# Kernel tuning notes

Hardware: AMD Instinct MI355X
Metric: run time of the kernel (lower is better)

Reference implementation:

```python
import jax, jax.numpy as jnp
import numpy as np

N_NODES = 100000
N_EDGES = 1600000
D_IN = 128
D_OUT = 128


def setup_inputs() -> dict:
    key = jax.random.key(0)
    k1, k2, k3, k4, k5 = jax.random.split(key, 5)
    x = jax.random.normal(k1, (N_NODES, D_IN), dtype=jnp.float32)
    # nn.Linear(in, out, bias=False) weight has shape [out, in]
    W = jax.random.normal(k2, (D_OUT, D_IN), dtype=jnp.float32) * (1.0 / np.sqrt(D_IN))
    edge_vals = jax.random.uniform(k3, (N_EDGES,), dtype=jnp.float32)
    edge_src = jax.random.randint(k4, (N_EDGES,), 0, N_NODES, dtype=jnp.int32)
    edge_dst = jax.random.randint(k5, (N_EDGES,), 0, N_NODES, dtype=jnp.int32)
    return {"x": x, "W": W, "edge_vals": edge_vals,
            "edge_src": edge_src, "edge_dst": edge_dst}


def reference(x, W, edge_vals, edge_src, edge_dst):
    # 1) linear projection (no bias): h = x @ W^T  -> [N, D_OUT]
    h = jnp.dot(x, W.T)
    # 2) sparse adjacency SpMM: out[i] = sum_{e: dst=i} vals[e] * h[src[e]]
    msgs = edge_vals[:, None] * h[edge_src]          # [E, D_OUT]
    agg = jax.ops.segment_sum(msgs, edge_dst, num_segments=N_NODES)
    # 3) exact GELU (torch.nn.GELU default)
    return jax.nn.gelu(agg, approximate=False)
```

## Files before the change

kernel.cpp:

```cpp
#include <hip/hip_runtime.h>
#include <math.h>

#define NN 100000
#define NE 1600000
#define D 128

#define NB 782
#define CAPB 2560
#define CURSTRIDE 16
#define SC_BLOCKS 512
#define SC_CHUNK 3125
#define SC_IT 13
#define CAP 1408

#define BM 64
#define GM_BLOCKS 1563
#define GRID (SC_BLOCKS + GM_BLOCKS)
#define TPAD 264

#define ASG __attribute__((address_space(1)))
#define ASL __attribute__((address_space(3)))

typedef __attribute__((ext_vector_type(8))) short bf16x8;
typedef __attribute__((ext_vector_type(4))) float f32x4;
typedef __attribute__((ext_vector_type(4))) unsigned int u32x4;

__device__ __forceinline__ unsigned int cvt_pk_bf16(float lo, float hi) {
    unsigned int r;
    asm("v_cvt_pk_bf16_f32 %0, %1, %2" : "=v"(r) : "v"(lo), "v"(hi));
    return r;
}

__device__ __forceinline__ unsigned int cvt_pk_f16(float lo, float hi) {
    auto p = __builtin_amdgcn_cvt_pkrtz(lo, hi);
    return __builtin_bit_cast(unsigned int, p);
}

__device__ __forceinline__ void fma_f16lo(float& acc, unsigned int h, float v) {
    asm("v_fma_mix_f32 %0, %1, %2, %0 op_sel:[0,0,0] op_sel_hi:[1,0,0]"
        : "+v"(acc) : "v"(h), "v"(v));
}
__device__ __forceinline__ void fma_f16hi(float& acc, unsigned int h, float v) {
    asm("v_fma_mix_f32 %0, %1, %2, %0 op_sel:[1,0,0] op_sel_hi:[1,0,0]"
        : "+v"(acc) : "v"(h), "v"(v));
}

__global__ __launch_bounds__(256) void wconv_kernel(const float* __restrict__ W,
                                                    unsigned short* __restrict__ Wswz,
                                                    int* __restrict__ bucketCursor) {
    int i = blockIdx.x * 256 + threadIdx.x;
    int r = i >> 4, s = i & 15;
    const float4* wp = reinterpret_cast<const float4*>(W + (size_t)r * D + s * 8);
    float4 v0 = wp[0], v1 = wp[1];
    uint2 a, b;
    a.x = cvt_pk_bf16(v0.x, v0.y); a.y = cvt_pk_bf16(v0.z, v0.w);
    b.x = cvt_pk_bf16(v1.x, v1.y); b.y = cvt_pk_bf16(v1.z, v1.w);
    int so = s ^ (r & 15);
    unsigned short* op = Wswz + (size_t)r * D + so * 8;
    *reinterpret_cast<uint2*>(op)     = a;
    *reinterpret_cast<uint2*>(op + 4) = b;
    for (int z = i; z < NB * CURSTRIDE; z += 2048) bucketCursor[z] = 0;
}

__global__ __launch_bounds__(256) void gemm_scatter_kernel(const float* __restrict__ x,
                                                           const unsigned short* __restrict__ Wswz,
                                                           unsigned short* __restrict__ h,
                                                           const int* __restrict__ src,
                                                           const int* __restrict__ dst,
                                                           const float* __restrict__ vals,
                                                           int* __restrict__ bucketCursor,
                                                           uint2* __restrict__ ebuf) {
    __shared__ __align__(16) unsigned char smem[40960];
    const int tid = threadIdx.x;
    const int lane = tid & 63;
    const int w = tid >> 6;
    const int g = blockIdx.x;

    if (g < SC_BLOCKS) {
        uint2* s_rec        = reinterpret_cast<uint2*>(smem);
        int*   l_off        = reinterpret_cast<int*>(smem + 25000);
        int*   l_cur        = reinterpret_cast<int*>(smem + 28128);
        int*   l_cnt        = reinterpret_cast<int*>(smem + 31256);
        int*   wtot         = reinterpret_cast<int*>(smem + 34384);
        unsigned short* s_b = reinterpret_cast<unsigned short*>(smem + 34400);

        const int t = tid;
        const int cb = g * SC_CHUNK;

        for (int i = t; i < NB; i += 256) l_cnt[i] = 0;
        __syncthreads();

        int dreg[SC_IT];
#pragma unroll
        for (int i = 0; i < SC_IT; ++i) {
            int o = t + 256 * i;
            dreg[i] = (o < SC_CHUNK) ? dst[cb + o] : -1;
            if (dreg[i] >= 0) atomicAdd(&l_cnt[dreg[i] >> 7], 1);
        }
        __syncthreads();

        int c[4];
        int s = 0;
#pragma unroll
        for (int i = 0; i < 4; ++i) {
            int b = 4 * t + i;
            c[i] = (b < NB) ? l_cnt[b] : 0;
            s += c[i];
        }
        int incl = s;
#pragma unroll
        for (int off = 1; off < 64; off <<= 1) {
            int v = __shfl_up(incl, off);
            if (lane >= off) incl += v;
        }
        if (lane == 63) wtot[w] = incl;
        __syncthreads();
        int run = incl - s;
        for (int k = 0; k < 4; ++k) if (k < w) run += wtot[k];
#pragma unroll
        for (int i = 0; i < 4; ++i) {
            int b = 4 * t + i;
            if (b < NB) {
                l_cur[b] = run;
                int gbase = b * CAPB +
                    (c[i] ? atomicAdd(&bucketCursor[b * CURSTRIDE], c[i]) : 0);
                l_off[b] = gbase - run;
            }
            run += c[i];
        }
        __syncthreads();

#pragma unroll
        for (int i = 0; i < SC_IT; ++i) {
            int o = t + 256 * i;
            if (dreg[i] >= 0) {
                int dn = dreg[i];
                int b = dn >> 7;
                uint2 rec;
                rec.x = (unsigned int)src[cb + o] | ((unsigned int)(dn & 127) << 17);
                rec.y = __float_as_uint(vals[cb + o]);
                int lofs = atomicAdd(&l_cur[b], 1);
                s_rec[lofs] = rec;
                s_b[lofs] = (unsigned short)b;
            }
        }
        __syncthreads();

#pragma unroll
        for (int i = 0; i < SC_IT; ++i) {
            int j = t + 256 * i;
            if (j < SC_CHUNK) {
                int b = s_b[j];
                ebuf[l_off[b] + j] = s_rec[j];
            }
        }
    } else {
        unsigned char* lBbuf = smem;
        const int rowBase = (g - SC_BLOCKS) * BM;

#pragma unroll
        for (int q = 0; q < 8; ++q) {
            const unsigned char* gp = reinterpret_cast<const unsigned char*>(Wswz)
                                      + (size_t)((w * 8 + q) * 1024 + lane * 16);
            unsigned char* lp = lBbuf + (w * 8 + q) * 1024;
            __builtin_amdgcn_global_load_lds((ASG const unsigned int*)(const void*)gp,
                                             (ASL unsigned int*)(void*)lp, 16, 0, 0);
        }

        const int l16 = lane & 15;
        const int arow = min(rowBase + w * 16 + l16, NN - 1);
        const float* xrow = x + (size_t)arow * D + (lane >> 4) * 8;

        bf16x8 afr[4];
#pragma unroll
        for (int kk = 0; kk < 4; ++kk) {
            float4 v0 = *reinterpret_cast<const float4*>(xrow + kk * 32);
            float4 v1 = *reinterpret_cast<const float4*>(xrow + kk * 32 + 4);
            u32x4 u;
            u[0] = cvt_pk_bf16(v0.x, v0.y);
            u[1] = cvt_pk_bf16(v0.z, v0.w);
            u[2] = cvt_pk_bf16(v1.x, v1.y);
            u[3] = cvt_pk_bf16(v1.z, v1.w);
            afr[kk] = __builtin_bit_cast(bf16x8, u);
        }
        __syncthreads();

        const int kx16 = (lane >> 4) * 16;
        f32x4 acc[8];
#pragma unroll
        for (int j = 0; j < 8; ++j) acc[j] = (f32x4){0.f, 0.f, 0.f, 0.f};

        const int bxor = l16 << 4;
#pragma unroll
        for (int kk = 0; kk < 4; ++kk) {
            int kbyte = kk * 64 + kx16;
#pragma unroll
            for (int j = 0; j < 8; ++j) {
                int row = j * 16 + l16;
                bf16x8 b = *reinterpret_cast<const bf16x8*>(
                    lBbuf + row * 256 + (kbyte ^ bxor));
                acc[j] = __builtin_amdgcn_mfma_f32_16x16x32_bf16(afr[kk], b, acc[j], 0, 0, 0);
            }
        }
        __syncthreads();

        const int lr0 = w * 16 + (lane >> 4) * 4;
#pragma unroll
        for (int j = 0; j < 8; ++j) {
            int col = j * 16 + l16;
            unsigned int d01 = cvt_pk_f16(acc[j][0], acc[j][1]);
            unsigned int d23 = cvt_pk_f16(acc[j][2], acc[j][3]);
            unsigned char* p0 = lBbuf + lr0 * TPAD + col * 2;
            *reinterpret_cast<unsigned short*>(p0)            = (unsigned short)d01;
            *reinterpret_cast<unsigned short*>(p0 + TPAD)     = (unsigned short)(d01 >> 16);
            *reinterpret_cast<unsigned short*>(p0 + 2 * TPAD) = (unsigned short)d23;
            *reinterpret_cast<unsigned short*>(p0 + 3 * TPAD) = (unsigned short)(d23 >> 16);
        }
        __syncthreads();

#pragma unroll
        for (int i = 0; i < 8; ++i) {
            int f = tid + 256 * i;
            int r = f >> 5, c = f & 31;
            if (rowBase + r < NN) {
                uint2 v = *reinterpret_cast<const uint2*>(lBbuf + r * TPAD + c * 8);
                *reinterpret_cast<uint2*>(reinterpret_cast<unsigned char*>(h)
                                          + (size_t)(rowBase + r) * 256 + c * 8) = v;
            }
        }
    }
}

__global__ __launch_bounds__(512) void pull_kernel(const unsigned short* __restrict__ h,
                                                   const int* __restrict__ bucketCursor,
                                                   const uint2* __restrict__ ebuf,
                                                   float* __restrict__ out) {
    __shared__ uint2 srec[CAP];
    __shared__ int cnt[64];
    __shared__ int start[65];
    __shared__ int cur[64];
    __shared__ __align__(16) unsigned char hbuf[8 * 4096];

    const int t = threadIdx.x;
    const int lane = t & 63;
    const int w = t >> 6;
    const int bid = blockIdx.x;
    const int b = bid >> 1;
    const int half = bid & 1;
    const int nodeBase = b * 128 + half * 64;

    unsigned char* hbufW = hbuf + w * 4096;

    float2 acc[8];
#pragma unroll
    for (int i = 0; i < 8; ++i) acc[i] = (float2){0.f, 0.f};

    const int n = min(bucketCursor[b * CURSTRIDE], CAPB);
    const uint2* eb = ebuf + (size_t)b * CAPB;

    if (t < 64) cnt[t] = 0;
    __syncthreads();

    uint2 rcache[5];
#pragma unroll
    for (int it = 0; it < 5; ++it) {
        int j = t + 512 * it;
        uint2 r = (j < n) ? eb[j] : (uint2){0xFFFFFFFFu, 0u};
        rcache[it] = r;
        if (j < n) {
            int dl = (int)((r.x >> 17) & 127);
            if ((dl >> 6) == half) atomicAdd(&cnt[dl & 63], 1);
        }
    }
    __syncthreads();

    if (w == 0) {
        int c = cnt[lane];
        int s = c;
        for (int off = 1; off < 64; off <<= 1) {
            int v = __shfl_up(s, off);
            if (lane >= off) s += v;
        }
        start[lane] = s - c;
        cur[lane] = s - c;
        if (lane == 63) start[64] = s;
    }
    __syncthreads();

#pragma unroll
    for (int it = 0; it < 5; ++it) {
        int j = t + 512 * it;
        if (j < n) {
            uint2 rec = rcache[it];
            int dl = (int)((rec.x >> 17) & 127);
            if ((dl >> 6) == half) {
                int p = atomicAdd(&cur[dl & 63], 1);
                srec[p] = rec;
            }
        }
    }
    __syncthreads();

    const int wbeg = start[w * 8];
    const int wend = start[w * 8 + 8];
    int issued = 0;
    int consumed = 0;

    auto issue_group = [&]() {
        int gbase = wbeg + issued * 8;
#pragma unroll
        for (int q = 0; q < 2; ++q) {
            int idx = min(gbase + q * 4 + (lane >> 4), wend - 1);
            unsigned int rx = reinterpret_cast<const unsigned int*>(&srec[idx])[0];
            const unsigned char* gp = reinterpret_cast<const unsigned char*>(h)
                                      + (size_t)(rx & 0x1FFFFu) * 256 + (size_t)((lane & 15) * 16);
            unsigned char* lp = hbufW + (issued & 1) * 2048 + q * 1024;
            __builtin_amdgcn_global_load_lds((ASG const unsigned int*)(const void*)gp,
                                             (ASL unsigned int*)(void*)lp, 16, 0, 0);
        }
        issued++;
    };

    if (wend > wbeg) { issue_group(); issue_group(); }

    int gate = wbeg;
    const unsigned char* slotcur = hbufW;
    const unsigned int* srec_dw = reinterpret_cast<const unsigned int*>(srec);

#pragma unroll
    for (int i = 0; i < 8; ++i) {
        const int s1 = start[w * 8 + i + 1];
        int e = start[w * 8 + i];
        float2 a = acc[i];
        while (e < s1) {
            if (e >= gate) {
                if (consumed) issue_group();
                asm volatile("s_waitcnt vmcnt(2)" ::: "memory");
                __builtin_amdgcn_sched_barrier(0);
                slotcur = hbufW + (consumed & 1) * 2048;
                consumed++;
                gate += 8;
            }
            const int lim = min(s1, gate);
            const unsigned char* hp = slotcur + ((e - wbeg) & 7) * 256 + lane * 4;
            for (; e + 1 < lim; e += 2) {
                unsigned int h0 = *reinterpret_cast<const unsigned int*>(hp);
                unsigned int h1 = *reinterpret_cast<const unsigned int*>(hp + 256);
                float v0 = __uint_as_float(srec_dw[e * 2 + 1]);
                float v1 = __uint_as_float(srec_dw[e * 2 + 3]);
                fma_f16lo(a.x, h0, v0);
                fma_f16hi(a.y, h0, v0);
                fma_f16lo(a.x, h1, v1);
                fma_f16hi(a.y, h1, v1);
                hp += 512;
            }
            if (e < lim) {
                unsigned int h0 = *reinterpret_cast<const unsigned int*>(hp);
                float v0 = __uint_as_float(srec_dw[e * 2 + 1]);
                fma_f16lo(a.x, h0, v0);
                fma_f16hi(a.y, h0, v0);
                ++e;
            }
        }
        acc[i] = a;
    }
    __syncthreads();

    const float is2 = 0.70710678118654752f;
#pragma unroll
    for (int i = 0; i < 8; ++i) {
        int node = nodeBase + w * 8 + i;
        if (node < NN) {
            float a0 = acc[i].x, a1 = acc[i].y;
            a0 = 0.5f * a0 * (1.f + erff(a0 * is2));
            a1 = 0.5f * a1 * (1.f + erff(a1 * is2));
            float2 o; o.x = a0; o.y = a1;
            *reinterpret_cast<float2*>(out + (size_t)node * D + lane * 2) = o;
        }
    }
}

extern "C" void kernel_launch(void* const* d_in, const int* in_sizes, int n_in,
                              void* d_out, int out_size, void* d_ws, size_t ws_size,
                              hipStream_t stream) {
    const float* x    = (const float*)d_in[0];
    const float* W    = (const float*)d_in[1];
    const float* vals = (const float*)d_in[2];
    const int*   src  = (const int*)d_in[3];
    const int*   dst  = (const int*)d_in[4];
    float* out = (float*)d_out;

    char* ws = (char*)d_ws;
    size_t off = 0;
    unsigned short* h    = (unsigned short*)(ws + off); off += (size_t)NN * D * 2;
    int* bucketCursor    = (int*)(ws + off);            off += (size_t)NB * CURSTRIDE * 4;
    off = (off + 15) & ~(size_t)15;
    unsigned short* Wswz = (unsigned short*)(ws + off); off += (size_t)D * D * 2;
    off = (off + 15) & ~(size_t)15;
    uint2* ebuf          = (uint2*)(ws + off);          off += (size_t)NB * CAPB * 8;

    wconv_kernel<<<8, 256, 0, stream>>>(W, Wswz, bucketCursor);
    gemm_scatter_kernel<<<GRID, 256, 0, stream>>>(
        x, Wswz, h, src, dst, vals, bucketCursor, ebuf);
    pull_kernel<<<NB * 2, 512, 0, stream>>>(h, bucketCursor, ebuf, out);
}
```

Measured before the change: 120.0 us.

## Bucket edges by 64-node half-buckets so pull blocks read only their own edges

The destination-bucket granularity of the scatter phase shrinks from 128 nodes to 64 nodes (1564 buckets), and scatter chunks become 2048 edges across 782 blocks. Each pull block now reads only the records of its own 64-node bucket. Before, both halves of a 128-node bucket read the whole bucket and filtered, so every edge record was loaded twice. The cost is more buckets, more global cursor atomics and a larger per-block prefix scan. Smaller per-bucket capacity (1280) also raises the risk of overflow for skewed degree distributions.

```diff
diff --git a/kernel.cpp b/kernel.cpp
--- a/kernel.cpp
+++ b/kernel.cpp
@@ -5,13 +5,13 @@
 #define NE 1600000
 #define D 128
 
-#define NB 782
-#define CAPB 2560
+#define NHB 1564
+#define CAPB 1280
 #define CURSTRIDE 16
-#define SC_BLOCKS 512
-#define SC_CHUNK 3125
-#define SC_IT 13
-#define CAP 1408
+#define SC_BLOCKS 782
+#define SC_CHUNK 2048
+#define SC_IT 8
+#define CAP 1280
 
 #define BM 64
 #define GM_BLOCKS 1563
@@ -59,7 +59,7 @@
     unsigned short* op = Wswz + (size_t)r * D + so * 8;
     *reinterpret_cast<uint2*>(op)     = a;
     *reinterpret_cast<uint2*>(op + 4) = b;
-    for (int z = i; z < NB * CURSTRIDE; z += 2048) bucketCursor[z] = 0;
+    for (int z = i; z < NHB * CURSTRIDE; z += 2048) bucketCursor[z] = 0;
 }
 
 __global__ __launch_bounds__(256) void gemm_scatter_kernel(const float* __restrict__ x,
@@ -78,33 +78,34 @@
 
     if (g < SC_BLOCKS) {
         uint2* s_rec        = reinterpret_cast<uint2*>(smem);
-        int*   l_off        = reinterpret_cast<int*>(smem + 25000);
-        int*   l_cur        = reinterpret_cast<int*>(smem + 28128);
-        int*   l_cnt        = reinterpret_cast<int*>(smem + 31256);
-        int*   wtot         = reinterpret_cast<int*>(smem + 34384);
-        unsigned short* s_b = reinterpret_cast<unsigned short*>(smem + 34400);
+        unsigned short* s_b = reinterpret_cast<unsigned short*>(smem + 16384);
+        int*   l_off        = reinterpret_cast<int*>(smem + 20480);
+        int*   l_cur        = reinterpret_cast<int*>(smem + 26736);
+        int*   l_cnt        = reinterpret_cast<int*>(smem + 32992);
+        int*   wtot         = reinterpret_cast<int*>(smem + 39248);
 
         const int t = tid;
         const int cb = g * SC_CHUNK;
 
-        for (int i = t; i < NB; i += 256) l_cnt[i] = 0;
+        for (int i = t; i < NHB; i += 256) l_cnt[i] = 0;
         __syncthreads();
 
         int dreg[SC_IT];
 #pragma unroll
         for (int i = 0; i < SC_IT; ++i) {
             int o = t + 256 * i;
-            dreg[i] = (o < SC_CHUNK) ? dst[cb + o] : -1;
-            if (dreg[i] >= 0) atomicAdd(&l_cnt[dreg[i] >> 7], 1);
-        }
-        __syncthreads();
-
-        int c[4];
+            int e = cb + o;
+            dreg[i] = (e < NE) ? dst[e] : -1;
+            if (dreg[i] >= 0) atomicAdd(&l_cnt[dreg[i] >> 6], 1);
+        }
+        __syncthreads();
+
+        int c[7];
         int s = 0;
 #pragma unroll
-        for (int i = 0; i < 4; ++i) {
-            int b = 4 * t + i;
-            c[i] = (b < NB) ? l_cnt[b] : 0;
+        for (int i = 0; i < 7; ++i) {
+            int b = 7 * t + i;
+            c[i] = (b < NHB) ? l_cnt[b] : 0;
             s += c[i];
         }
         int incl = s;
@@ -118,9 +119,9 @@
         int run = incl - s;
         for (int k = 0; k < 4; ++k) if (k < w) run += wtot[k];
 #pragma unroll
-        for (int i = 0; i < 4; ++i) {
-            int b = 4 * t + i;
-            if (b < NB) {
+        for (int i = 0; i < 7; ++i) {
+            int b = 7 * t + i;
+            if (b < NHB) {
                 l_cur[b] = run;
                 int gbase = b * CAPB +
                     (c[i] ? atomicAdd(&bucketCursor[b * CURSTRIDE], c[i]) : 0);
@@ -135,9 +136,9 @@
             int o = t + 256 * i;
             if (dreg[i] >= 0) {
                 int dn = dreg[i];
-                int b = dn >> 7;
+                int b = dn >> 6;
                 uint2 rec;
-                rec.x = (unsigned int)src[cb + o] | ((unsigned int)(dn & 127) << 17);
+                rec.x = (unsigned int)src[cb + o] | ((unsigned int)(dn & 63) << 17);
                 rec.y = __float_as_uint(vals[cb + o]);
                 int lofs = atomicAdd(&l_cur[b], 1);
                 s_rec[lofs] = rec;
@@ -146,10 +147,11 @@
         }
         __syncthreads();
 
+        const int nloc = min(SC_CHUNK, NE - cb);
 #pragma unroll
         for (int i = 0; i < SC_IT; ++i) {
             int j = t + 256 * i;
-            if (j < SC_CHUNK) {
+            if (j < nloc) {
                 int b = s_b[j];
                 ebuf[l_off[b] + j] = s_rec[j];
             }
@@ -244,10 +246,8 @@
     const int t = threadIdx.x;
     const int lane = t & 63;
     const int w = t >> 6;
-    const int bid = blockIdx.x;
-    const int b = bid >> 1;
-    const int half = bid & 1;
-    const int nodeBase = b * 128 + half * 64;
+    const int hb = blockIdx.x;
+    const int nodeBase = hb * 64;
 
     unsigned char* hbufW = hbuf + w * 4096;
 
@@ -255,22 +255,19 @@
 #pragma unroll
     for (int i = 0; i < 8; ++i) acc[i] = (float2){0.f, 0.f};
 
-    const int n = min(bucketCursor[b * CURSTRIDE], CAPB);
-    const uint2* eb = ebuf + (size_t)b * CAPB;
+    const int n = min(bucketCursor[hb * CURSTRIDE], CAPB);
+    const uint2* eb = ebuf + (size_t)hb * CAPB;
 
     if (t < 64) cnt[t] = 0;
     __syncthreads();
 
-    uint2 rcache[5];
-#pragma unroll
-    for (int it = 0; it < 5; ++it) {
+    uint2 rcache[3];
+#pragma unroll
+    for (int it = 0; it < 3; ++it) {
         int j = t + 512 * it;
         uint2 r = (j < n) ? eb[j] : (uint2){0xFFFFFFFFu, 0u};
         rcache[it] = r;
-        if (j < n) {
-            int dl = (int)((r.x >> 17) & 127);
-            if ((dl >> 6) == half) atomicAdd(&cnt[dl & 63], 1);
-        }
+        if (j < n) atomicAdd(&cnt[(r.x >> 17) & 63], 1);
     }
     __syncthreads();
 
@@ -288,15 +285,12 @@
     __syncthreads();
 
 #pragma unroll
-    for (int it = 0; it < 5; ++it) {
+    for (int it = 0; it < 3; ++it) {
         int j = t + 512 * it;
         if (j < n) {
             uint2 rec = rcache[it];
-            int dl = (int)((rec.x >> 17) & 127);
-            if ((dl >> 6) == half) {
-                int p = atomicAdd(&cur[dl & 63], 1);
-                srec[p] = rec;
-            }
+            int p = atomicAdd(&cur[(rec.x >> 17) & 63], 1);
+            srec[p] = rec;
         }
     }
     __syncthreads();
@@ -393,14 +387,14 @@
     char* ws = (char*)d_ws;
     size_t off = 0;
     unsigned short* h    = (unsigned short*)(ws + off); off += (size_t)NN * D * 2;
-    int* bucketCursor    = (int*)(ws + off);            off += (size_t)NB * CURSTRIDE * 4;
+    int* bucketCursor    = (int*)(ws + off);            off += (size_t)NHB * CURSTRIDE * 4;
     off = (off + 15) & ~(size_t)15;
     unsigned short* Wswz = (unsigned short*)(ws + off); off += (size_t)D * D * 2;
     off = (off + 15) & ~(size_t)15;
-    uint2* ebuf          = (uint2*)(ws + off);          off += (size_t)NB * CAPB * 8;
+    uint2* ebuf          = (uint2*)(ws + off);          off += (size_t)NHB * CAPB * 8;
 
     wconv_kernel<<<8, 256, 0, stream>>>(W, Wswz, bucketCursor);
     gemm_scatter_kernel<<<GRID, 256, 0, stream>>>(
         x, Wswz, h, src, dst, vals, bucketCursor, ebuf);
-    pull_kernel<<<NB * 2, 512, 0, stream>>>(h, bucketCursor, ebuf, out);
-}
+    pull_kernel<<<NHB, 512, 0, stream>>>(h, bucketCursor, ebuf, out);
+}
```

After: 157.8 us. 31.5% more time.
